# Kernel optimization log

Measured on AMD Instinct MI355X. Metric: run time of the kernel, lower is better.

## Reference

```python
import jax, jax.numpy as jnp
import numpy as np

N = 100000   # nodes
E = 1600000  # edges
D = 64       # hidden_channels
H = 2 * D    # MLP expansion
L = 4        # num_layers
G = 64       # graphs in batch
OUT = 1      # out_channels
LN_EPS = 1e-5


def layer_norm(h, gamma, beta):
    mu = jnp.mean(h, axis=-1, keepdims=True)
    var = jnp.var(h, axis=-1, keepdims=True)
    return (h - mu) * jax.lax.rsqrt(var + LN_EPS) * gamma + beta


def setup_inputs() -> dict:
    key = jax.random.key(0)
    ks = jax.random.split(key, 16)
    s = 0.05
    x = jax.random.normal(ks[0], (N, D), jnp.float32)
    edge_index = jax.random.randint(ks[1], (2, E), 0, N)
    batch = jnp.sort(jax.random.randint(ks[2], (N,), 0, G))
    # lin_in
    W_in = jax.random.normal(ks[3], (D, D), jnp.float32) * s
    b_in = jnp.zeros((D,), jnp.float32)
    # per-layer GINConv params (stacked over L layers)
    eps = jnp.zeros((L,), jnp.float32)
    W1 = jax.random.normal(ks[4], (L, D, H), jnp.float32) * s
    b1 = jnp.zeros((L, H), jnp.float32)
    gamma = jnp.ones((L, H), jnp.float32)
    beta = jnp.zeros((L, H), jnp.float32)
    W2 = jax.random.normal(ks[5], (L, H, D), jnp.float32) * s
    b2 = jnp.zeros((L, D), jnp.float32)
    # lin_out MLP
    Wo1 = jax.random.normal(ks[6], (D, H), jnp.float32) * s
    bo1 = jnp.zeros((H,), jnp.float32)
    Wo2 = jax.random.normal(ks[7], (H, OUT), jnp.float32) * s
    bo2 = jnp.zeros((OUT,), jnp.float32)
    return {
        "x": x, "W_in": W_in, "b_in": b_in, "eps": eps,
        "W1": W1, "b1": b1, "gamma": gamma, "beta": beta,
        "W2": W2, "b2": b2, "Wo1": Wo1, "bo1": bo1,
        "Wo2": Wo2, "bo2": bo2,
        "edge_index": edge_index, "batch": batch,
    }


def gin_conv(h, edge_index, eps_l, W1_l, b1_l, gamma_l, beta_l, W2_l, b2_l):
    src = edge_index[0]  # x_j
    dst = edge_index[1]  # aggregation target i
    # message = relu(x_j); aggr = scatter-add into dst
    agg = jax.ops.segment_sum(jax.nn.relu(h[src]), dst, num_segments=N)
    z = (1.0 + eps_l) * h + agg
    z = z @ W1_l + b1_l
    z = jax.nn.relu(layer_norm(z, gamma_l, beta_l))
    return z @ W2_l + b2_l


def reference(x, W_in, b_in, eps, W1, b1, gamma, beta, W2, b2,
              Wo1, bo1, Wo2, bo2, edge_index, batch):
    h = x @ W_in + b_in  # [N, D]
    for i in range(L):
        h = h + gin_conv(h, edge_index, eps[i], W1[i], b1[i],
                         gamma[i], beta[i], W2[i], b2[i])
        # dropout p=0.0 -> identity
    pooled = jax.ops.segment_sum(h, batch, num_segments=G)  # [G, D]
    out = jax.nn.relu(pooled @ Wo1 + bo1) @ Wo2 + bo2        # [G, OUT]
    return out.reshape(-1)
```

## Files before the change

kernel.cpp:

```cpp
#include <hip/hip_runtime.h>
#include <hip/hip_bf16.h>

#define NN 100000
#define NE 1600000
#define DD 64
#define HH 128
#define NLAYERS 4
#define NGRAPH 64
#define NBUCKET 782
#define CHUNKSZ 8192
#define NCHUNK 196
#define NTOT (NBUCKET * NCHUNK)

typedef __attribute__((ext_vector_type(8))) short bf16x8;
typedef __attribute__((ext_vector_type(4))) float f32x4;
typedef __attribute__((ext_vector_type(2))) float f32x2;

__device__ inline unsigned short bf16bits(float v) {
  return __bfloat16_as_ushort(__float2bfloat16(v));
}
__device__ inline float lo16(unsigned int u) { return __uint_as_float(u << 16); }
__device__ inline float hi16(unsigned int u) { return __uint_as_float(u & 0xFFFF0000u); }
__device__ inline float b2f(unsigned short u) { return __uint_as_float(((unsigned int)u) << 16); }
__device__ inline unsigned char f8byte(float v) {
  int pk = __builtin_amdgcn_cvt_pk_fp8_f32(fmaxf(v, 0.f), 0.f, 0, false);
  return (unsigned char)(pk & 0xFF);
}


__global__ void k_hist(const int* __restrict__ dst, int* __restrict__ hist) {
  __shared__ int lh[NBUCKET];
  int t = threadIdx.x;
  int blk = blockIdx.x;
  for (int i = t; i < NBUCKET; i += 256) lh[i] = 0;
  __syncthreads();
  int cb = blk * CHUNKSZ;
  int end = min(cb + CHUNKSZ, NE);
  for (int i = cb + t; i < end; i += 256)
    atomicAdd(&lh[dst[i] >> 7], 1);
  __syncthreads();
  for (int i = t; i < NBUCKET; i += 256)
    hist[i * NCHUNK + blk] = lh[i];
}

__global__ void k_scan1(const int* __restrict__ in, int* __restrict__ out,
                        int* __restrict__ bsum, int n) {
  __shared__ int s[256];
  int t = threadIdx.x;
  int i = blockIdx.x * 256 + t;
  int v = (i < n) ? in[i] : 0;
  s[t] = v;
  __syncthreads();
  for (int off = 1; off < 256; off <<= 1) {
    int x = (t >= off) ? s[t - off] : 0;
    __syncthreads();
    s[t] += x;
    __syncthreads();
  }
  if (i < n) out[i] = s[t] - v;
  if (t == 255) bsum[blockIdx.x] = s[255];
}

__global__ void k_scan2b(int* bsum, int nb) {
  __shared__ int s[256];
  int t = threadIdx.x;
  int base = t * 5;
  int v[5];
  int sum = 0;
#pragma unroll
  for (int j = 0; j < 5; j++) {
    int i = base + j;
    v[j] = (i < nb) ? bsum[i] : 0;
    sum += v[j];
  }
  s[t] = sum;
  __syncthreads();
  for (int off = 1; off < 256; off <<= 1) {
    int x = (t >= off) ? s[t - off] : 0;
    __syncthreads();
    s[t] += x;
    __syncthreads();
  }
  int ex = s[t] - sum;
#pragma unroll
  for (int j = 0; j < 5; j++) {
    int i = base + j;
    if (i < nb) { int vv = v[j]; bsum[i] = ex; ex += vv; }
  }
}

__global__ void k_scan3b(int* __restrict__ hist, const int* __restrict__ bsum,
                         int* __restrict__ bbase, int n) {
  int i = blockIdx.x * 256 + threadIdx.x;
  if (i < n) {
    int v = hist[i] + bsum[i >> 8];
    hist[i] = v;
    if (i % NCHUNK == 0) bbase[i / NCHUNK] = v;
  }
}

__global__ void k_scatter(const int* __restrict__ src, const int* __restrict__ dst,
                          const int* __restrict__ hist, unsigned int* __restrict__ tmp) {
  __shared__ int lcur[NBUCKET];
  int t = threadIdx.x;
  int blk = blockIdx.x;
  for (int i = t; i < NBUCKET; i += 256) lcur[i] = hist[i * NCHUNK + blk];
  __syncthreads();
  int cb = blk * CHUNKSZ;
  int end = min(cb + CHUNKSZ, NE);
  for (int i = cb + t; i < end; i += 256) {
    int d = dst[i];
    int pos = atomicAdd(&lcur[d >> 7], 1);
    tmp[pos] = ((unsigned int)(d & 127) << 20) | (unsigned int)src[i];
  }
}

__global__ void k_fillB2(const unsigned int* __restrict__ tmp,
                         const int* __restrict__ bbase,
                         int* __restrict__ csr, int* __restrict__ offs,
                         int* __restrict__ cnt) {
  __shared__ int lcnt[128], lex[128], lcur[128];
  int b = blockIdx.x;
  int t = threadIdx.x;
  int base = bbase[b];
  int end = (b == NBUCKET - 1) ? NE : bbase[b + 1];
  if (t < 128) lcnt[t] = 0;
  __syncthreads();
  for (int i = base + t; i < end; i += 256)
    atomicAdd(&lcnt[tmp[i] >> 20], 1);
  __syncthreads();
  int v = (t < 128) ? lcnt[t] : 0;
  if (t < 128) lex[t] = v;
  __syncthreads();
  for (int off = 1; off < 128; off <<= 1) {
    int x = (t >= off && t < 128) ? lex[t - off] : 0;
    __syncthreads();
    if (t < 128) lex[t] += x;
    __syncthreads();
  }
  if (t < 128) {
    int ex = lex[t] - v;
    lcur[t] = ex;
    int node = (b << 7) + t;
    if (node < NN) { offs[node] = base + ex; cnt[node] = v; }
  }
  __syncthreads();
  for (int i = base + t; i < end; i += 256) {
    unsigned int u = tmp[i];
    int dl = u >> 20;
    int pos = atomicAdd(&lcur[dl], 1);
    csr[base + pos] = u & 0xFFFFF;
  }
}

__global__ void k_prep(const float* __restrict__ W1, const float* __restrict__ W2,
                       const float* __restrict__ W_in,
                       unsigned short* __restrict__ W1t, unsigned short* __restrict__ W2t,
                       unsigned short* __restrict__ Wint) {
  int bidx = blockIdx.x;
  int t = threadIdx.x;
  if (bidx == 2 * NLAYERS) {
    for (int i = t; i < 4096; i += 256) {
      int c = i >> 6, k = i & 63;
      Wint[i] = bf16bits(W_in[k * 64 + c]);
    }
    return;
  }
  int l = bidx >> 1;
  int m = bidx & 1;
  if (m == 0) {
    const float* src = W1 + (size_t)l * 8192;
    unsigned short* dstp = W1t + (size_t)l * 8192;
    for (int i = t; i < 8192; i += 256) {
      int c = i >> 6, k = i & 63;
      dstp[i] = bf16bits(src[k * 128 + c]);
    }
  } else {
    const float* src = W2 + (size_t)l * 8192;
    unsigned short* dstp = W2t + (size_t)l * 8192;
    for (int i = t; i < 8192; i += 256) {
      int c = i >> 7, k = i & 127;
      dstp[i] = bf16bits(src[k * 64 + c]);
    }
  }
}

__global__ __launch_bounds__(256) void k_lin(
    const float* __restrict__ x, const unsigned short* __restrict__ Wint,
    const float* __restrict__ binp, unsigned short* __restrict__ hout,
    unsigned char* __restrict__ f8out) {
  __shared__ __align__(16) unsigned short sW[4096];
  __shared__ float sb[64];
  int t = threadIdx.x;
  {
    const uint4* wg = (const uint4*)Wint;
    uint4* sWu = (uint4*)sW;
    for (int g = t; g < 512; g += 256) {
      int c = g >> 3, s = g & 7;
      sWu[c * 8 + (s ^ (c & 7))] = wg[g];
    }
    if (t < 64) sb[t] = binp[t];
  }
  int l = t & 63, w = t >> 6, lm = l & 15, lk = l >> 4;
  int rowl = w * 16 + lm;
  int grow = blockIdx.x * 64 + rowl;
  int growc = min(grow, NN - 1);
  bf16x8 a[2];
#pragma unroll
  for (int kb = 0; kb < 2; kb++) {
    const float* xp = &x[(size_t)growc * 64 + kb * 32 + lk * 8];
    float4 x0 = *(const float4*)xp;
    float4 x1 = *(const float4*)(xp + 4);
    a[kb][0] = (short)bf16bits(x0.x); a[kb][1] = (short)bf16bits(x0.y);
    a[kb][2] = (short)bf16bits(x0.z); a[kb][3] = (short)bf16bits(x0.w);
    a[kb][4] = (short)bf16bits(x1.x); a[kb][5] = (short)bf16bits(x1.y);
    a[kb][6] = (short)bf16bits(x1.z); a[kb][7] = (short)bf16bits(x1.w);
  }
  __syncthreads();
  f32x4 acc[4];
#pragma unroll
  for (int n = 0; n < 4; n++) {
    float bc = sb[n * 16 + lm];
    acc[n] = (f32x4){bc, bc, bc, bc};
  }
  const bf16x8* sWf = (const bf16x8*)sW;
#pragma unroll
  for (int n = 0; n < 4; n++) {
    int c = n * 16 + lm;
    bf16x8 b0 = sWf[c * 8 + ((0 * 4 + lk) ^ (c & 7))];
    bf16x8 b1 = sWf[c * 8 + ((1 * 4 + lk) ^ (c & 7))];
    acc[n] = __builtin_amdgcn_mfma_f32_16x16x32_bf16(a[0], b0, acc[n], 0, 0, 0);
    acc[n] = __builtin_amdgcn_mfma_f32_16x16x32_bf16(a[1], b1, acc[n], 0, 0, 0);
  }
#pragma unroll
  for (int r = 0; r < 4; r++) {
    int grow2 = blockIdx.x * 64 + w * 16 + lk * 4 + r;
    if (grow2 < NN) {
#pragma unroll
      for (int n = 0; n < 4; n++) {
        int c = n * 16 + lm;
        size_t idx = (size_t)grow2 * 64 + c;
        float o = acc[n][r];
        hout[idx] = bf16bits(o);
        f8out[idx] = f8byte(o);
      }
    }
  }
}

__global__ __launch_bounds__(256) void k_fused(
    unsigned short* __restrict__ h, const uint2* __restrict__ f8in,
    unsigned char* __restrict__ f8out,
    const int* __restrict__ csr, const int* __restrict__ offs,
    const int* __restrict__ cnt,
    const unsigned short* __restrict__ W1t, const float* __restrict__ b1l,
    const float* __restrict__ gl, const float* __restrict__ btl,
    const unsigned short* __restrict__ W2t, const float* __restrict__ b2l,
    const float* __restrict__ epsl) {
  __shared__ __align__(16) unsigned short sW[8192];
  __shared__ __align__(16) unsigned short sRr[8192];
  __shared__ float sb1[128], sg[128], sbt[128], sb2[64];

  int t = threadIdx.x;
  int nbase = blockIdx.x * 64;
  int l = t & 63;
  int w = t >> 6;
  int lm = l & 15;
  int lk = l >> 4;

  {
    const uint4* w1g = (const uint4*)W1t;
    uint4* sWu = (uint4*)sW;
    for (int g = t; g < 1024; g += 256) {
      int c = g >> 3, s = g & 7;
      sWu[c * 8 + (s ^ (c & 7))] = w1g[g];
    }
    if (t < 128) { sb1[t] = b1l[t]; sg[t] = gl[t]; sbt[t] = btl[t]; }
    if (t < 64) sb2[t] = b2l[t];
  }
  float epsv = 1.0f + *epsl;

  int rowl = w * 16 + lm;
  int grow = nbase + rowl;
  int growc = min(grow, NN - 1);
  int start = offs[growc];
  int deg = (grow < NN) ? cnt[growc] : 0;

  const unsigned short* hp = h + (size_t)growc * 64 + lk * 8;
  uint4 hva = *(const uint4*)hp;
  uint4 hvb = *(const uint4*)(hp + 32);

  float accA[8] = {0.f, 0.f, 0.f, 0.f, 0.f, 0.f, 0.f, 0.f};
  float accB[8] = {0.f, 0.f, 0.f, 0.f, 0.f, 0.f, 0.f, 0.f};
  for (int j0 = 0; j0 < deg; j0 += 8) {
    int idxA = csr[start + j0 + lk];
    int idxB = csr[start + j0 + 4 + lk];
    int c8 = deg - j0;
    int ss[8];
#pragma unroll
    for (int jj = 0; jj < 4; jj++) ss[jj] = __shfl(idxA, lm + jj * 16);
#pragma unroll
    for (int jj = 0; jj < 4; jj++) ss[4 + jj] = __shfl(idxB, lm + jj * 16);
    uint2 va[8], vb[8];
#pragma unroll
    for (int jj = 0; jj < 8; jj++) {
      int s = (jj < c8) ? ss[jj] : ss[0];
      va[jj] = f8in[(size_t)s * 8 + lk];
      vb[jj] = f8in[(size_t)s * 8 + 4 + lk];
    }
#pragma unroll
    for (int jj = 0; jj < 8; jj++) {
      if (jj < c8) {
        f32x2 p;
        p = __builtin_amdgcn_cvt_pk_f32_fp8(va[jj].x, false); accA[0] += p.x; accA[1] += p.y;
        p = __builtin_amdgcn_cvt_pk_f32_fp8(va[jj].x, true);  accA[2] += p.x; accA[3] += p.y;
        p = __builtin_amdgcn_cvt_pk_f32_fp8(va[jj].y, false); accA[4] += p.x; accA[5] += p.y;
        p = __builtin_amdgcn_cvt_pk_f32_fp8(va[jj].y, true);  accA[6] += p.x; accA[7] += p.y;
        p = __builtin_amdgcn_cvt_pk_f32_fp8(vb[jj].x, false); accB[0] += p.x; accB[1] += p.y;
        p = __builtin_amdgcn_cvt_pk_f32_fp8(vb[jj].x, true);  accB[2] += p.x; accB[3] += p.y;
        p = __builtin_amdgcn_cvt_pk_f32_fp8(vb[jj].y, false); accB[4] += p.x; accB[5] += p.y;
        p = __builtin_amdgcn_cvt_pk_f32_fp8(vb[jj].y, true);  accB[6] += p.x; accB[7] += p.y;
      }
    }
  }

  bf16x8 a1[2];
  {
    float hz[8];
    hz[0] = lo16(hva.x); hz[1] = hi16(hva.x); hz[2] = lo16(hva.y); hz[3] = hi16(hva.y);
    hz[4] = lo16(hva.z); hz[5] = hi16(hva.z); hz[6] = lo16(hva.w); hz[7] = hi16(hva.w);
#pragma unroll
    for (int j = 0; j < 8; j++) a1[0][j] = (short)bf16bits(epsv * hz[j] + accA[j]);
    hz[0] = lo16(hvb.x); hz[1] = hi16(hvb.x); hz[2] = lo16(hvb.y); hz[3] = hi16(hvb.y);
    hz[4] = lo16(hvb.z); hz[5] = hi16(hvb.z); hz[6] = lo16(hvb.w); hz[7] = hi16(hvb.w);
#pragma unroll
    for (int j = 0; j < 8; j++) a1[1][j] = (short)bf16bits(epsv * hz[j] + accB[j]);
  }
  __syncthreads();

  f32x4 acc1[8];
#pragma unroll
  for (int n = 0; n < 8; n++) {
    float bc = sb1[n * 16 + lm];
    acc1[n] = (f32x4){bc, bc, bc, bc};
  }
  {
    const bf16x8* sW1f = (const bf16x8*)sW;
#pragma unroll
    for (int n = 0; n < 8; n++) {
      int c = n * 16 + lm;
      bf16x8 b0 = sW1f[c * 8 + ((0 * 4 + lk) ^ (c & 7))];
      bf16x8 b1f = sW1f[c * 8 + ((1 * 4 + lk) ^ (c & 7))];
      acc1[n] = __builtin_amdgcn_mfma_f32_16x16x32_bf16(a1[0], b0, acc1[n], 0, 0, 0);
      acc1[n] = __builtin_amdgcn_mfma_f32_16x16x32_bf16(a1[1], b1f, acc1[n], 0, 0, 0);
    }
  }

  float psr[4], pqr[4];
#pragma unroll
  for (int r = 0; r < 4; r++) {
    float s = 0.f, q = 0.f;
#pragma unroll
    for (int n = 0; n < 8; n++) { float v = acc1[n][r]; s += v; q += v * v; }
    psr[r] = s; pqr[r] = q;
  }
#pragma unroll
  for (int m = 1; m <= 8; m <<= 1) {
#pragma unroll
    for (int r = 0; r < 4; r++) {
      psr[r] += __shfl_xor(psr[r], m);
      pqr[r] += __shfl_xor(pqr[r], m);
    }
  }
#pragma unroll
  for (int r = 0; r < 4; r++) {
    float mu = psr[r] * (1.0f / 128.0f);
    float var = pqr[r] * (1.0f / 128.0f) - mu * mu;
    float rs = rsqrtf(var + 1e-5f);
    int rowr = w * 16 + lk * 4 + r;
#pragma unroll
    for (int n = 0; n < 8; n++) {
      int c = n * 16 + lm;
      float v = (acc1[n][r] - mu) * rs * sg[c] + sbt[c];
      v = fmaxf(v, 0.f);
      int slot = (c >> 3) ^ (rowr & 7);
      sRr[rowr * 128 + slot * 8 + (c & 7)] = bf16bits(v);
    }
  }
  __syncthreads();

  {
    const uint4* w2g = (const uint4*)W2t;
    uint4* sWu = (uint4*)sW;
    for (int g = t; g < 1024; g += 256) {
      int c = g >> 4, s = g & 15;
      sWu[c * 16 + (s ^ (c & 15))] = w2g[g];
    }
  }
  __syncthreads();

  f32x4 acc2[4];
#pragma unroll
  for (int n2 = 0; n2 < 4; n2++) {
    float bc = sb2[n2 * 16 + lm];
    acc2[n2] = (f32x4){bc, bc, bc, bc};
  }
  {
    const bf16x8* sRf = (const bf16x8*)sRr;
    const bf16x8* sW2f = (const bf16x8*)sW;
    bf16x8 a2[4];
#pragma unroll
    for (int kb = 0; kb < 4; kb++)
      a2[kb] = sRf[rowl * 16 + ((kb * 4 + lk) ^ (rowl & 7))];
#pragma unroll
    for (int n2 = 0; n2 < 4; n2++) {
      int c = n2 * 16 + lm;
#pragma unroll
      for (int kb = 0; kb < 4; kb++) {
        bf16x8 bfr = sW2f[c * 16 + ((kb * 4 + lk) ^ (c & 15))];
        acc2[n2] = __builtin_amdgcn_mfma_f32_16x16x32_bf16(a2[kb], bfr, acc2[n2], 0, 0, 0);
      }
    }
  }

#pragma unroll
  for (int r = 0; r < 4; r++) {
    int grow2 = nbase + w * 16 + lk * 4 + r;
    if (grow2 < NN) {
#pragma unroll
      for (int n2 = 0; n2 < 4; n2++) {
        int c = n2 * 16 + lm;
        size_t idx = (size_t)grow2 * 64 + c;
        float o = b2f(h[idx]) + acc2[n2][r];
        h[idx] = bf16bits(o);
        f8out[idx] = f8byte(o);
      }
    }
  }
}

__global__ void k_pool(const unsigned short* __restrict__ h,
                       const int* __restrict__ batch,
                       float* __restrict__ pooled, int n) {
  int t = threadIdx.x;
  int d = t & 63;
  int w = t >> 6;
  int n0 = blockIdx.x * 256 + w * 64;
  float acc = 0.f;
  int prev = -1;
  for (int i = 0; i < 64; i++) {
    int nn = n0 + i;
    if (nn >= n) break;
    int g = batch[nn];
    if (g != prev) {
      if (prev >= 0) atomicAdd(&pooled[prev * 64 + d], acc);
      prev = g;
      acc = 0.f;
    }
    acc += b2f(h[(size_t)nn * 64 + d]);
  }
  if (prev >= 0) atomicAdd(&pooled[prev * 64 + d], acc);
}

__global__ __launch_bounds__(128) void k_out(
    const float* __restrict__ pooled, const float* __restrict__ Wo1,
    const float* __restrict__ bo1, const float* __restrict__ Wo2,
    const float* __restrict__ bo2, float* __restrict__ out) {
  __shared__ __align__(16) float sP[64];
  __shared__ float sPart[2];
  int g = blockIdx.x;
  int c = threadIdx.x;
  if (c < 64) sP[c] = pooled[g * 64 + c];
  __syncthreads();
  float t1 = bo1[c];
#pragma unroll 8
  for (int k = 0; k < 64; k++) t1 += sP[k] * Wo1[k * 128 + c];
  float v = fmaxf(t1, 0.f) * Wo2[c];
#pragma unroll
  for (int m = 1; m <= 32; m <<= 1) v += __shfl_xor(v, m);
  if ((c & 63) == 0) sPart[c >> 6] = v;
  __syncthreads();
  if (c == 0) out[g] = sPart[0] + sPart[1] + bo2[0];
}


static inline char* align_up(char* p, size_t a) {
  return (char*)(((uintptr_t)p + a - 1) & ~(uintptr_t)(a - 1));
}

extern "C" void kernel_launch(void* const* d_in, const int* in_sizes, int n_in,
                              void* d_out, int out_size, void* d_ws, size_t ws_size,
                              hipStream_t stream) {
  const float* x    = (const float*)d_in[0];
  const float* W_in = (const float*)d_in[1];
  const float* b_in = (const float*)d_in[2];
  const float* eps  = (const float*)d_in[3];
  const float* W1   = (const float*)d_in[4];
  const float* b1   = (const float*)d_in[5];
  const float* gam  = (const float*)d_in[6];
  const float* bet  = (const float*)d_in[7];
  const float* W2   = (const float*)d_in[8];
  const float* b2   = (const float*)d_in[9];
  const float* Wo1  = (const float*)d_in[10];
  const float* bo1  = (const float*)d_in[11];
  const float* Wo2  = (const float*)d_in[12];
  const float* bo2  = (const float*)d_in[13];
  const int* ei     = (const int*)d_in[14];
  const int* batch  = (const int*)d_in[15];
  float* out = (float*)d_out;

  const int* e_src = ei;
  const int* e_dst = ei + NE;

  char* p = (char*)d_ws;
  unsigned short* h = (unsigned short*)p;   p += (size_t)NN * 64 * 2;
  unsigned char* f8A = (unsigned char*)p;   p += (size_t)NN * 64;
  unsigned char* f8B = (unsigned char*)p;
  unsigned int* tmp = (unsigned int*)p;
                                            p += (size_t)NN * 64;
  int* csr = (int*)p;
  int* hist = (int*)p;
                                            p += (size_t)NE * 4;
  int* offs = (int*)p;                      p += (size_t)NN * 4;
  int* cnt = (int*)p;                       p += (size_t)NN * 4;
  int* bsumH = (int*)p;                     p += 1280 * 4;
  int* bbase = (int*)p;                     p += (NBUCKET + 1) * 4;
  p = align_up(p, 256);
  float* pooled = (float*)p;                p += (size_t)NGRAPH * 64 * 4;
  p = align_up(p, 256);
  unsigned short* W1t = (unsigned short*)p; p += (size_t)NLAYERS * 8192 * 2;
  unsigned short* W2t = (unsigned short*)p; p += (size_t)NLAYERS * 8192 * 2;
  unsigned short* Wint = (unsigned short*)p; p += 4096 * 2;

  const int SCAN_BLOCKS_H = (NTOT + 255) / 256;
  const int NODE_BLOCKS = (NN + 63) / 64;

  hipMemsetAsync(pooled, 0, (size_t)NGRAPH * 64 * 4, stream);

  k_hist<<<NCHUNK, 256, 0, stream>>>(e_dst, hist);
  k_scan1<<<SCAN_BLOCKS_H, 256, 0, stream>>>(hist, hist, bsumH, NTOT);
  k_scan2b<<<1, 256, 0, stream>>>(bsumH, SCAN_BLOCKS_H);
  k_scan3b<<<SCAN_BLOCKS_H, 256, 0, stream>>>(hist, bsumH, bbase, NTOT);
  k_scatter<<<NCHUNK, 256, 0, stream>>>(e_src, e_dst, hist, tmp);
  k_fillB2<<<NBUCKET, 256, 0, stream>>>(tmp, bbase, csr, offs, cnt);

  k_prep<<<NLAYERS * 2 + 1, 256, 0, stream>>>(W1, W2, W_in, W1t, W2t, Wint);
  k_lin<<<NODE_BLOCKS, 256, 0, stream>>>(x, Wint, b_in, h, f8A);

  for (int l = 0; l < NLAYERS; l++) {
    const uint2* fin = (const uint2*)((l & 1) ? f8B : f8A);
    unsigned char* fout = (l & 1) ? f8A : f8B;
    k_fused<<<NODE_BLOCKS, 256, 0, stream>>>(h, fin, fout, csr, offs, cnt,
        W1t + (size_t)l * 8192, b1 + (size_t)l * 128,
        gam + (size_t)l * 128, bet + (size_t)l * 128,
        W2t + (size_t)l * 8192, b2 + (size_t)l * 64,
        eps + l);
  }

  k_pool<<<(NN + 255) / 256, 256, 0, stream>>>(h, batch, pooled, NN);
  k_out<<<NGRAPH, 128, 0, stream>>>(pooled, Wo1, bo1, Wo2, bo2, out);
}
```

Baseline: 314.5 us.

## Sort nodes by in-degree so fused layer blocks process degree-balanced rows

Adds a counting sort of nodes by in-degree (histogram, scan, scatter) that builds a permutation. The fused GIN layer kernel then assigns rows through this permutation, so each wavefront gathers neighbours for nodes with similar degree and its per-lane loop trip counts diverge less. The cost is five extra small preprocessing launches and indirect, non-contiguous row accesses for h and the fp8 output in the fused kernel.

Result: slower. 334.3 us (+6.3%).

```diff
diff --git a/kernel.cpp b/kernel.cpp
--- a/kernel.cpp
+++ b/kernel.cpp
@@ -11,6 +11,9 @@
 #define CHUNKSZ 8192
 #define NCHUNK 196
 #define NTOT (NBUCKET * NCHUNK)
+#define NCHN 391
+#define NBIN 64
+#define NTOTD (NBIN * NCHN)
 
 typedef __attribute__((ext_vector_type(8))) short bf16x8;
 typedef __attribute__((ext_vector_type(4))) float f32x4;
@@ -99,6 +102,11 @@
   }
 }
 
+__global__ void k_scan3c(int* __restrict__ arr, const int* __restrict__ bsum, int n) {
+  int i = blockIdx.x * 256 + threadIdx.x;
+  if (i < n) arr[i] += bsum[i >> 8];
+}
+
 __global__ void k_scatter(const int* __restrict__ src, const int* __restrict__ dst,
                           const int* __restrict__ hist, unsigned int* __restrict__ tmp) {
   __shared__ int lcur[NBUCKET];
@@ -150,6 +158,30 @@
     int dl = u >> 20;
     int pos = atomicAdd(&lcur[dl], 1);
     csr[base + pos] = u & 0xFFFFF;
+  }
+}
+
+__global__ void k_dhist(const int* __restrict__ cnt, int* __restrict__ dh) {
+  __shared__ int lh[NBIN];
+  int t = threadIdx.x, blk = blockIdx.x;
+  if (t < NBIN) lh[t] = 0;
+  __syncthreads();
+  int node = blk * 256 + t;
+  if (node < NN) atomicAdd(&lh[min(cnt[node], NBIN - 1)], 1);
+  __syncthreads();
+  if (t < NBIN) dh[t * NCHN + blk] = lh[t];
+}
+
+__global__ void k_dscatter(const int* __restrict__ cnt, const int* __restrict__ dh,
+                           int* __restrict__ perm) {
+  __shared__ int lcur[NBIN];
+  int t = threadIdx.x, blk = blockIdx.x;
+  if (t < NBIN) lcur[t] = dh[t * NCHN + blk];
+  __syncthreads();
+  int node = blk * 256 + t;
+  if (node < NN) {
+    int pos = atomicAdd(&lcur[min(cnt[node], NBIN - 1)], 1);
+    perm[pos] = node;
   }
 }
 
@@ -250,7 +282,7 @@
 
 __global__ __launch_bounds__(256) void k_fused(
     unsigned short* __restrict__ h, const uint2* __restrict__ f8in,
-    unsigned char* __restrict__ f8out,
+    unsigned char* __restrict__ f8out, const int* __restrict__ perm,
     const int* __restrict__ csr, const int* __restrict__ offs,
     const int* __restrict__ cnt,
     const unsigned short* __restrict__ W1t, const float* __restrict__ b1l,
@@ -283,10 +315,11 @@
   int rowl = w * 16 + lm;
   int grow = nbase + rowl;
   int growc = min(grow, NN - 1);
-  int start = offs[growc];
-  int deg = (grow < NN) ? cnt[growc] : 0;
-
-  const unsigned short* hp = h + (size_t)growc * 64 + lk * 8;
+  int node = perm[growc];
+  int start = offs[node];
+  int deg = (grow < NN) ? cnt[node] : 0;
+
+  const unsigned short* hp = h + (size_t)node * 64 + lk * 8;
   uint4 hva = *(const uint4*)hp;
   uint4 hvb = *(const uint4*)(hp + 32);
 
@@ -427,10 +460,11 @@
   for (int r = 0; r < 4; r++) {
     int grow2 = nbase + w * 16 + lk * 4 + r;
     if (grow2 < NN) {
+      int node2 = perm[grow2];
 #pragma unroll
       for (int n2 = 0; n2 < 4; n2++) {
         int c = n2 * 16 + lm;
-        size_t idx = (size_t)grow2 * 64 + c;
+        size_t idx = (size_t)node2 * 64 + c;
         float o = b2f(h[idx]) + acc2[n2][r];
         h[idx] = bf16bits(o);
         f8out[idx] = f8byte(o);
@@ -523,7 +557,10 @@
                                             p += (size_t)NE * 4;
   int* offs = (int*)p;                      p += (size_t)NN * 4;
   int* cnt = (int*)p;                       p += (size_t)NN * 4;
+  int* perm = (int*)p;                      p += (size_t)NN * 4;
+  int* dh = (int*)p;                        p += (size_t)NTOTD * 4;
   int* bsumH = (int*)p;                     p += 1280 * 4;
+  int* bsumD = (int*)p;                     p += 128 * 4;
   int* bbase = (int*)p;                     p += (NBUCKET + 1) * 4;
   p = align_up(p, 256);
   float* pooled = (float*)p;                p += (size_t)NGRAPH * 64 * 4;
@@ -533,6 +570,7 @@
   unsigned short* Wint = (unsigned short*)p; p += 4096 * 2;
 
   const int SCAN_BLOCKS_H = (NTOT + 255) / 256;
+  const int SCAN_BLOCKS_D = (NTOTD + 255) / 256;
   const int NODE_BLOCKS = (NN + 63) / 64;
 
   hipMemsetAsync(pooled, 0, (size_t)NGRAPH * 64 * 4, stream);
@@ -544,13 +582,19 @@
   k_scatter<<<NCHUNK, 256, 0, stream>>>(e_src, e_dst, hist, tmp);
   k_fillB2<<<NBUCKET, 256, 0, stream>>>(tmp, bbase, csr, offs, cnt);
 
+  k_dhist<<<NCHN, 256, 0, stream>>>(cnt, dh);
+  k_scan1<<<SCAN_BLOCKS_D, 256, 0, stream>>>(dh, dh, bsumD, NTOTD);
+  k_scan2b<<<1, 256, 0, stream>>>(bsumD, SCAN_BLOCKS_D);
+  k_scan3c<<<SCAN_BLOCKS_D, 256, 0, stream>>>(dh, bsumD, NTOTD);
+  k_dscatter<<<NCHN, 256, 0, stream>>>(cnt, dh, perm);
+
   k_prep<<<NLAYERS * 2 + 1, 256, 0, stream>>>(W1, W2, W_in, W1t, W2t, Wint);
   k_lin<<<NODE_BLOCKS, 256, 0, stream>>>(x, Wint, b_in, h, f8A);
 
   for (int l = 0; l < NLAYERS; l++) {
     const uint2* fin = (const uint2*)((l & 1) ? f8B : f8A);
     unsigned char* fout = (l & 1) ? f8A : f8B;
-    k_fused<<<NODE_BLOCKS, 256, 0, stream>>>(h, fin, fout, csr, offs, cnt,
+    k_fused<<<NODE_BLOCKS, 256, 0, stream>>>(h, fin, fout, perm, csr, offs, cnt,
         W1t + (size_t)l * 8192, b1 + (size_t)l * 128,
         gam + (size_t)l * 128, bet + (size_t)l * 128,
         W2t + (size_t)l * 8192, b2 + (size_t)l * 64,
```
